# Optimization experiments

Measured on AMD Instinct MI355X. Metric: run time of the kernel, lower is better.

## Reference

```python
import jax, jax.numpy as jnp
import numpy as np

RADIUS = 0.1
NSAMPLE = 32


def _ball_query(new_xyz, xyz, radius, nsample):
    # new_xyz: (B, S, 3), xyz: (B, N, 3) -> idx (B, S, nsample) int32
    N = xyz.shape[1]
    d2 = jnp.sum((new_xyz[:, :, None, :] - xyz[:, None, :, :]) ** 2, axis=-1)  # (B,S,N)
    mask = d2 < radius * radius
    cand = jnp.where(mask, jnp.arange(N, dtype=jnp.int32)[None, None, :], N)
    cand = jnp.sort(cand, axis=-1)[:, :, :nsample]  # first nsample in-ball indices
    first = cand[:, :, :1]
    first = jnp.where(first == N, 0, first)  # empty ball -> index 0 (CUDA semantics)
    return jnp.where(cand == N, first, cand).astype(jnp.int32)


def _group(features, idx):
    # features: (B, C, N), idx: (B, S, K) -> (B, C, S, K)
    return jax.vmap(lambda f, i: f[:, i])(features, idx)


def setup_inputs() -> dict:
    key = jax.random.key(0)
    k1, k2, k3, k4 = jax.random.split(key, 4)
    B, N, S, C = 4, 16384, 2048, 64
    xyz = jax.random.uniform(k1, (B, N, 3), dtype=jnp.float32)
    new_xyz = jax.random.uniform(k2, (B, S, 3), dtype=jnp.float32)
    features = jax.random.normal(k3, (B, C, N), dtype=jnp.float32)
    fps_idx = jax.random.randint(k4, (B, S), 0, N, dtype=jnp.int32)
    return {"xyz": xyz, "new_xyz": new_xyz, "features": features, "fps_idx": fps_idx}


def reference(xyz, new_xyz, features, fps_idx):
    idx = _ball_query(new_xyz, xyz, RADIUS, NSAMPLE)          # (B,S,nsample)
    idx = jnp.concatenate([fps_idx[:, :, None], idx], axis=2)  # (B,S,nsample+1)
    xyz_t = jnp.transpose(xyz, (0, 2, 1))                      # (B,3,N)
    raw_grouped_xyz = _group(xyz_t, idx)                       # (B,3,S,K)
    grouped_xyz = raw_grouped_xyz - jnp.transpose(new_xyz, (0, 2, 1))[..., None]
    grouped_features = _group(features, idx)                   # (B,C,S,K)
    return jnp.concatenate([raw_grouped_xyz, grouped_xyz, grouped_features], axis=1)
```

## Files before the change

kernel.cpp:

```cpp
#include <hip/hip_runtime.h>

#define BB 4
#define NN 16384
#define SS 2048
#define CC 64
#define NS 32
#define KK 33
#define OC 70
#define SCH 4
#define GT 512
#define NC 10
#define NCELL 1000
#define HCAP 224
#define RPAD 0.100001f

__device__ __forceinline__ float sq_nofma(float v) {
  float r = v * v;
  asm volatile("" : "+v"(r));
  return r;
}

__device__ __forceinline__ int cell1(float x) {
  int c = (int)(x * 10.0f);
  return c < 0 ? 0 : (c > 9 ? 9 : c);
}
__device__ __forceinline__ int cell3(float x, float y, float z) {
  return (cell1(z) * NC + cell1(y)) * NC + cell1(x);
}

__device__ __forceinline__ void ball_query_wave(
    const float* __restrict__ xb, float qx, float qy, float qz, int lane,
    int* out) {
  const float R2 = 0.01f;
  int cnt = 0;
  int firstIdx = 0;
  for (int base = 0; base < NN; base += 256) {
    float px[4], py[4], pz[4];
#pragma unroll
    for (int j = 0; j < 4; ++j) {
      int n = base + j * 64 + lane;
      const float* p = xb + n * 3;
      px[j] = p[0]; py[j] = p[1]; pz[j] = p[2];
    }
#pragma unroll
    for (int j = 0; j < 4; ++j) {
      float dx = px[j] - qx, dy = py[j] - qy, dz = pz[j] - qz;
      float d2 = sq_nofma(dx) + sq_nofma(dy);
      asm volatile("" : "+v"(d2));
      d2 = d2 + sq_nofma(dz);
      bool m = d2 < R2;
      unsigned long long bal = __ballot(m);
      if (cnt == 0 && bal) firstIdx = base + j * 64 + __builtin_ctzll(bal);
      int pos = cnt + (int)__popcll(bal & ((1ull << lane) - 1ull));
      if (m && pos < NS) out[pos] = base + j * 64 + lane;
      cnt += (int)__popcll(bal);
    }
    if (cnt >= NS) break;
  }
  if (cnt < NS) {
    int pad = (cnt == 0) ? 0 : firstIdx;
    if (lane >= cnt && lane < NS) out[lane] = pad;
  }
}

__global__ __launch_bounds__(256) void qg_tr_hist2(
    const float* __restrict__ xyz, const float* __restrict__ feat,
    float* __restrict__ featT, int* __restrict__ partial) {
  __shared__ float tile[32 * 260];
  __shared__ int h[1024];
  const int bid = (int)blockIdx.x;
  const int tid = (int)threadIdx.x;
  const int b = bid >> 7;
  const int rest = bid & 127;
  const int n0 = (rest >> 1) << 8;
  const int cc = rest & 1;
  const int c0 = cc << 5;
  const int wv = tid >> 6, lane = tid & 63;

  if (cc == 0) {
#pragma unroll
    for (int c = tid; c < 1024; c += 256) h[c] = 0;
    __syncthreads();
    const float* p = xyz + ((size_t)b * NN + n0 + tid) * 3;
    atomicAdd(&h[cell3(p[0], p[1], p[2])], 1);
  }

  const float* fb = feat + ((size_t)b * CC + c0) * NN + n0;
#pragma unroll
  for (int rr = 0; rr < 8; ++rr) {
    int c = rr * 4 + wv;
    float4 v = *(const float4*)(fb + (size_t)c * NN + 4 * lane);
    *(float4*)&tile[c * 260 + 4 * lane] = v;
  }
  __syncthreads();
  const int c4 = lane & 7, m = lane >> 3;
  float4* oT = (float4*)(featT + ((size_t)b * NN + n0) * CC);
#pragma unroll
  for (int it = 0; it < 8; ++it) {
    int n = it * 32 + wv * 8 + m;
    float4 v;
    v.x = tile[(4 * c4 + 0) * 260 + n];
    v.y = tile[(4 * c4 + 1) * 260 + n];
    v.z = tile[(4 * c4 + 2) * 260 + n];
    v.w = tile[(4 * c4 + 3) * 260 + n];
    oT[(size_t)n * (CC / 4) + (c0 >> 2) + c4] = v;
  }

  if (cc == 0) {
    const int j = rest >> 1;
    int* pr = partial + (((size_t)b * 128 + j) << 10);
#pragma unroll
    for (int c = tid; c < 1024; c += 256) pr[c] = h[c];
  }
}

__global__ __launch_bounds__(256) void qg_scan2(
    const int* __restrict__ partial, int* __restrict__ off,
    int* __restrict__ woff) {
  __shared__ int sc[256];
  const int b = (int)blockIdx.x;
  const int tid = (int)threadIdx.x;
  int l0 = 0, l1 = 0, l2 = 0, l3 = 0;
  for (int j = 0; j < 64; j += 4) {
#pragma unroll
    for (int jj = 0; jj < 4; ++jj) {
      const int4 v = ((const int4*)(partial + (((size_t)b * 128 + j + jj) << 10)))[tid];
      l0 += v.x; l1 += v.y; l2 += v.z; l3 += v.w;
    }
  }
  int base = tid * 4;
  int s1 = l0, s2 = l0 + l1, s3 = l0 + l1 + l2, tot = s3 + l3;
  sc[tid] = tot;
  __syncthreads();
  for (int d = 1; d < 256; d <<= 1) {
    int v = (tid >= d) ? sc[tid - d] : 0;
    __syncthreads();
    sc[tid] += v;
    __syncthreads();
  }
  int ex = sc[tid] - tot;
  int* offb = off + b * (NCELL + 1);
  int* woffb = woff + b * NCELL;
  if (base + 0 < NCELL) { offb[base + 0] = ex;      woffb[base + 0] = ex; }
  if (base + 1 < NCELL) { offb[base + 1] = ex + s1; woffb[base + 1] = ex + s1; }
  if (base + 2 < NCELL) { offb[base + 2] = ex + s2; woffb[base + 2] = ex + s2; }
  if (base + 3 < NCELL) { offb[base + 3] = ex + s3; woffb[base + 3] = ex + s3; }
  if (tid == 0) offb[NCELL] = NN;
}

__global__ __launch_bounds__(256) void qg_scatter(
    const float* __restrict__ xyz, int* __restrict__ woff,
    float4* __restrict__ pts) {
  int i = (int)(blockIdx.x * 256u + threadIdx.x);
  int b = i >> 14, n = i & (NN - 1);
  const float* p = xyz + ((size_t)b * NN + n) * 3;
  float x = p[0], y = p[1], z = p[2];
  int cell = cell3(x, y, z);
  int pos = atomicAdd(&woff[b * NCELL + cell], 1);
  pts[(b << 14) + pos] = make_float4(x, y, z, __int_as_float(n));
}

__global__ __launch_bounds__(GT) void qg_main(
    const float* __restrict__ xyz, const float* __restrict__ nxyz,
    const float4* __restrict__ pts, const int* __restrict__ off,
    const float* __restrict__ featT, const int* __restrict__ fps,
    float* __restrict__ out) {
  __shared__ float sf[CC][SCH * KK + 1];
  __shared__ int sidx[SCH * KK];
  __shared__ int hitbuf[SCH][HCAP];
  __shared__ int hcnt_s[SCH];
  const int tid = (int)threadIdx.x;
  const int blk = (int)blockIdx.x;
  const int b = blk >> 9;
  const int s0 = (blk & 511) * SCH;
  const int wv = tid >> 6, lane = tid & 63;

  if (wv < SCH) {
    const int q = b * SS + s0 + wv;
    const float R2 = 0.01f;
    float qx = nxyz[q * 3 + 0];
    float qy = nxyz[q * 3 + 1];
    float qz = nxyz[q * 3 + 2];
    int* hb = hitbuf[wv];
    int* qout = &sidx[wv * KK];
    if (lane == 0) hcnt_s[wv] = 0;
    asm volatile("s_waitcnt lgkmcnt(0)" ::: "memory");

    int lox = max(0, (int)floorf((qx - RPAD) * 10.f));
    int hix = min(9, (int)floorf((qx + RPAD) * 10.f));
    int loy = max(0, (int)floorf((qy - RPAD) * 10.f));
    int hiy = min(9, (int)floorf((qy + RPAD) * 10.f));
    int loz = max(0, (int)floorf((qz - RPAD) * 10.f));
    int hiz = min(9, (int)floorf((qz + RPAD) * 10.f));

    const int* offb = off + b * (NCELL + 1);
    int start_l = 0, end_l = 0;
    {
      int cz = loz + lane / 3, cy = loy + lane % 3;
      if (lane < 9 && cz <= hiz && cy <= hiy) {
        int row = (cz * NC + cy) * NC;
        start_l = offb[row + lox];
        end_l = offb[row + hix + 1];
      }
    }
    const float4* pb = pts + ((size_t)b << 14);
    for (int sp = 0; sp < 9; ++sp) {
      int start = __shfl(start_l, sp, 64);
      int end = __shfl(end_l, sp, 64);
      for (int p0 = start; p0 < end; p0 += 64) {
        int ii = p0 + lane;
        bool valid = ii < end;
        float4 v = pb[valid ? ii : (end - 1)];
        float dx = v.x - qx, dy = v.y - qy, dz = v.z - qz;
        float d2 = sq_nofma(dx) + sq_nofma(dy);
        asm volatile("" : "+v"(d2));
        d2 = d2 + sq_nofma(dz);
        if (valid && d2 < R2) {
          int pos = atomicAdd(&hcnt_s[wv], 1);
          if (pos < HCAP) hb[pos] = __float_as_int(v.w);
        }
      }
    }
    asm volatile("s_waitcnt lgkmcnt(0)" ::: "memory");
    const int M = hcnt_s[wv];
    if (M > HCAP) {
      ball_query_wave(xyz + (size_t)b * NN * 3, qx, qy, qz, lane, qout + 1);
    } else {
      int minv = 0x7fffffff;
      for (int i = lane; i < M; i += 64) {
        int hh = hb[i];
        minv = min(minv, hh);
        int rank = 0;
        for (int j = 0; j < M; ++j) rank += (hb[j] < hh) ? 1 : 0;
        if (rank < NS) qout[1 + rank] = hh;
      }
      if (M < NS) {
#pragma unroll
        for (int d = 1; d < 64; d <<= 1)
          minv = min(minv, __shfl_xor(minv, d, 64));
        int pad = (M == 0) ? 0 : minv;
        if (lane >= M && lane < NS) qout[1 + lane] = pad;
      }
    }
    if (lane == 0) qout[0] = fps[q];
  }
  __syncthreads();

  const size_t cstr = (size_t)SS * KK;
  const float4* fT4 = (const float4*)(featT + (size_t)b * NN * CC);
  int e = tid & 15;
  for (int pp = tid >> 4; pp < SCH * KK; pp += GT / 16) {
    int n = sidx[pp];
    float4 v = fT4[(size_t)n * (CC / 4) + e];
    sf[4 * e + 0][pp] = v.x;
    sf[4 * e + 1][pp] = v.y;
    sf[4 * e + 2][pp] = v.z;
    sf[4 * e + 3][pp] = v.w;
  }

  if (tid < SCH * KK) {
    int s4 = tid / KK;
    int n = sidx[tid];
    const float* p = xyz + ((size_t)b * NN + n) * 3;
    float x = p[0], y = p[1], z = p[2];
    int q = b * SS + s0 + s4;
    float cx = nxyz[q * 3 + 0], cy = nxyz[q * 3 + 1], cz = nxyz[q * 3 + 2];
    size_t obase = ((size_t)(b * OC) * SS + s0) * KK + tid;
    out[obase + 0 * cstr] = x;
    out[obase + 1 * cstr] = y;
    out[obase + 2 * cstr] = z;
    out[obase + 3 * cstr] = x - cx;
    out[obase + 4 * cstr] = y - cy;
    out[obase + 5 * cstr] = z - cz;
  }
  __syncthreads();

  size_t fbase = ((size_t)(b * OC + 6) * SS + s0) * KK;
  for (int idx = tid; idx < CC * SCH * KK; idx += GT) {
    int c = idx / (SCH * KK);
    int j = idx - c * (SCH * KK);
    out[fbase + (size_t)c * cstr + j] = sf[c][j];
  }
}

__global__ __launch_bounds__(256) void qg_prep(
    const float* __restrict__ xyz, const float* __restrict__ nxyz,
    const float* __restrict__ feat, int* __restrict__ wsidx,
    float* __restrict__ featT) {
  __shared__ float tile[64][65];
  int bid = (int)blockIdx.x;
  int r3 = bid % 3;
  if (r3 < 2) {
    int lane = (int)(threadIdx.x & 63);
    int q = ((bid / 3) * 2 + r3) * 4 + (int)(threadIdx.x >> 6);
    int b = q >> 11;
    const float* xb = xyz + (size_t)b * NN * 3;
    ball_query_wave(xb, nxyz[q * 3], nxyz[q * 3 + 1], nxyz[q * 3 + 2], lane,
                    wsidx + (size_t)q * NS);
  } else {
    int tb = bid / 3;
    int b = tb >> 8;
    int n0 = (tb & 255) << 6;
    int tx = (int)(threadIdx.x & 63);
    int ty = (int)(threadIdx.x >> 6);
    const float* fb = feat + (size_t)b * CC * NN + n0;
#pragma unroll
    for (int r = 0; r < 16; ++r) {
      int c = r * 4 + ty;
      tile[c][tx] = fb[(size_t)c * NN + tx];
    }
    __syncthreads();
    float* ob = featT + ((size_t)b * NN + n0) * CC;
#pragma unroll
    for (int r = 0; r < 16; ++r) {
      int n = r * 4 + ty;
      ob[(size_t)n * CC + tx] = tile[tx][n];
    }
  }
}

__global__ __launch_bounds__(GT) void qg_gather2(
    const float* __restrict__ xyz, const float* __restrict__ nxyz,
    const float* __restrict__ featT, const int* __restrict__ fps,
    const int* __restrict__ wsidx, float* __restrict__ out) {
  __shared__ float sf[CC][SCH * KK + 1];
  __shared__ int sidx[SCH * KK];
  const int tid = (int)threadIdx.x;
  const int blk = (int)blockIdx.x;
  const int b = blk >> 9;
  const int s0 = (blk & 511) * SCH;
  const size_t cstr = (size_t)SS * KK;

  if (tid < SCH * KK) {
    int s4 = tid / KK, k = tid - s4 * KK;
    int q = b * SS + s0 + s4;
    sidx[tid] = (k == 0) ? fps[q] : wsidx[(size_t)q * NS + (k - 1)];
  }
  __syncthreads();

  const float4* fT4 = (const float4*)(featT + (size_t)b * NN * CC);
  int e = tid & 15;
  for (int pp = tid >> 4; pp < SCH * KK; pp += GT / 16) {
    int n = sidx[pp];
    float4 v = fT4[(size_t)n * (CC / 4) + e];
    sf[4 * e + 0][pp] = v.x;
    sf[4 * e + 1][pp] = v.y;
    sf[4 * e + 2][pp] = v.z;
    sf[4 * e + 3][pp] = v.w;
  }

  if (tid < SCH * KK) {
    int s4 = tid / KK;
    int n = sidx[tid];
    const float* p = xyz + ((size_t)b * NN + n) * 3;
    float x = p[0], y = p[1], z = p[2];
    int q = b * SS + s0 + s4;
    float cx = nxyz[q * 3 + 0], cy = nxyz[q * 3 + 1], cz = nxyz[q * 3 + 2];
    size_t obase = ((size_t)(b * OC) * SS + s0) * KK + tid;
    out[obase + 0 * cstr] = x;
    out[obase + 1 * cstr] = y;
    out[obase + 2 * cstr] = z;
    out[obase + 3 * cstr] = x - cx;
    out[obase + 4 * cstr] = y - cy;
    out[obase + 5 * cstr] = z - cz;
  }
  __syncthreads();

  size_t fbase = ((size_t)(b * OC + 6) * SS + s0) * KK;
  for (int idx = tid; idx < CC * SCH * KK; idx += GT) {
    int c = idx / (SCH * KK);
    int j = idx - c * (SCH * KK);
    out[fbase + (size_t)c * cstr + j] = sf[c][j];
  }
}

__global__ __launch_bounds__(256) void qg_ballq(
    const float* __restrict__ xyz, const float* __restrict__ nxyz,
    int* __restrict__ wsidx) {
  int q = (int)((blockIdx.x * blockDim.x + threadIdx.x) >> 6);
  int lane = (int)(threadIdx.x & 63);
  int b = q / SS;
  const float* xb = xyz + (size_t)b * NN * 3;
  ball_query_wave(xb, nxyz[q * 3], nxyz[q * 3 + 1], nxyz[q * 3 + 2], lane,
                  wsidx + (size_t)q * NS);
}

__global__ __launch_bounds__(256) void qg_gather(
    const float* __restrict__ xyz, const float* __restrict__ nxyz,
    const float* __restrict__ feat, const int* __restrict__ fps,
    const int* __restrict__ wsidx, float* __restrict__ out) {
  unsigned t = blockIdx.x * 256u + threadIdx.x;
  const unsigned TOT = (unsigned)BB * OC * SS * KK;
  if (t >= TOT) return;
  unsigned k = t % KK;
  unsigned r = t / KK;
  unsigned s = r % SS;
  r /= SS;
  unsigned c = r % OC;
  unsigned b = r / OC;
  unsigned q = b * SS + s;
  int n = (k == 0) ? fps[q] : wsidx[(size_t)q * NS + (k - 1)];
  float v;
  if (c < 6) {
    unsigned cc = (c < 3) ? c : c - 3;
    v = xyz[((size_t)b * NN + (unsigned)n) * 3 + cc];
    if (c >= 3) v -= nxyz[q * 3 + cc];
  } else {
    v = feat[((size_t)b * CC + (c - 6)) * NN + (unsigned)n];
  }
  out[t] = v;
}

__global__ __launch_bounds__(256) void qg_fused(
    const float* __restrict__ xyz, const float* __restrict__ nxyz,
    const float* __restrict__ feat, const int* __restrict__ fps,
    float* __restrict__ out) {
  __shared__ int sidx[4][KK];
  int wv = (int)(threadIdx.x >> 6), lane = (int)(threadIdx.x & 63);
  int q = (int)blockIdx.x * 4 + wv;
  int b = q / SS, s = q % SS;
  const float* xb = xyz + (size_t)b * NN * 3;
  ball_query_wave(xb, nxyz[q * 3], nxyz[q * 3 + 1], nxyz[q * 3 + 2], lane,
                  &sidx[wv][1]);
  if (lane == 0) sidx[wv][0] = fps[q];
  __syncthreads();
  for (int f = lane; f < OC * KK; f += 64) {
    int c = f / KK, k = f - c * KK;
    int n = sidx[wv][k];
    float v;
    if (c < 6) {
      int cc = (c < 3) ? c : c - 3;
      v = xb[n * 3 + cc];
      if (c >= 3) v -= nxyz[q * 3 + cc];
    } else {
      v = feat[((size_t)b * CC + (c - 6)) * NN + n];
    }
    out[((size_t)((size_t)b * OC + c) * SS + s) * KK + k] = v;
  }
}

extern "C" void kernel_launch(void* const* d_in, const int* in_sizes, int n_in,
                              void* d_out, int out_size, void* d_ws, size_t ws_size,
                              hipStream_t stream) {
  const float* xyz  = (const float*)d_in[0];
  const float* nxyz = (const float*)d_in[1];
  const float* feat = (const float*)d_in[2];
  const int*   fps  = (const int*)d_in[3];
  float* out = (float*)d_out;

  const size_t pts_b     = (size_t)BB * NN * sizeof(float4);
  const size_t off_b     = 16384;
  const size_t partial_b = (size_t)BB * 128 * 1024 * sizeof(int);
  const size_t woff_b    = 16384;
  const size_t featT_b   = (size_t)BB * NN * CC * sizeof(float);
  const size_t grid_need = pts_b + off_b + partial_b + woff_b + featT_b;

  const size_t idx_b = (size_t)BB * SS * NS * sizeof(int);

  if (ws_size >= grid_need) {
    char* w = (char*)d_ws;
    float4* pts     = (float4*)w;                    w += pts_b;
    int*    off     = (int*)w;                       w += off_b;
    int*    partial = (int*)w;                       w += partial_b;
    int*    woff    = (int*)w;                       w += woff_b;
    float*  featT   = (float*)w;
    qg_tr_hist2<<<512, 256, 0, stream>>>(xyz, feat, featT, partial);
    qg_scan2<<<BB, 256, 0, stream>>>(partial, off, woff);
    qg_scatter<<<(BB * NN) / 256, 256, 0, stream>>>(xyz, woff, pts);
    qg_main<<<BB * (SS / SCH), GT, 0, stream>>>(xyz, nxyz, pts, off, featT,
                                                fps, out);
  } else if (ws_size >= idx_b + featT_b) {
    int* wsidx = (int*)d_ws;
    float* featT = (float*)((char*)d_ws + idx_b);
    qg_prep<<<3072, 256, 0, stream>>>(xyz, nxyz, feat, wsidx, featT);
    qg_gather2<<<BB * (SS / SCH), GT, 0, stream>>>(xyz, nxyz, featT, fps,
                                                   wsidx, out);
  } else if (ws_size >= idx_b) {
    int* wsidx = (int*)d_ws;
    qg_ballq<<<(BB * SS) / 4, 256, 0, stream>>>(xyz, nxyz, wsidx);
    unsigned tot = (unsigned)BB * OC * SS * KK;
    qg_gather<<<(tot + 255u) / 256u, 256, 0, stream>>>(xyz, nxyz, feat, fps,
                                                       wsidx, out);
  } else {
    qg_fused<<<(BB * SS) / 4, 256, 0, stream>>>(xyz, nxyz, feat, fps, out);
  }
}
```

Measured before the change: 55.26 us.

## Split fused grid query+gather kernel into separate query and gather kernels

The fused qg_main kernel, which did the cell-grid ball query in 4 of 8 waves and then the feature gather, is split in two. A 256-thread qg_query kernel writes neighbour indices to a new workspace buffer, and the existing qg_gather2 kernel then does the gather. This is meant to stop half the 512-thread block idling during the query and to let each phase run at its own occupancy. The cost is an extra kernel launch plus an index round trip through global memory. The second fallback path also loses the qg_prep route and now uses qg_ballq with qg_gather.

```diff
diff --git a/kernel.cpp b/kernel.cpp
--- a/kernel.cpp
+++ b/kernel.cpp
@@ -160,162 +160,79 @@
   pts[(b << 14) + pos] = make_float4(x, y, z, __int_as_float(n));
 }
 
-__global__ __launch_bounds__(GT) void qg_main(
+__global__ __launch_bounds__(256) void qg_query(
     const float* __restrict__ xyz, const float* __restrict__ nxyz,
     const float4* __restrict__ pts, const int* __restrict__ off,
-    const float* __restrict__ featT, const int* __restrict__ fps,
-    float* __restrict__ out) {
-  __shared__ float sf[CC][SCH * KK + 1];
-  __shared__ int sidx[SCH * KK];
-  __shared__ int hitbuf[SCH][HCAP];
-  __shared__ int hcnt_s[SCH];
+    int* __restrict__ wsidx) {
+  __shared__ int hitbuf[4][HCAP];
+  __shared__ int hcnt_s[4];
   const int tid = (int)threadIdx.x;
-  const int blk = (int)blockIdx.x;
-  const int b = blk >> 9;
-  const int s0 = (blk & 511) * SCH;
   const int wv = tid >> 6, lane = tid & 63;
-
-  if (wv < SCH) {
-    const int q = b * SS + s0 + wv;
-    const float R2 = 0.01f;
-    float qx = nxyz[q * 3 + 0];
-    float qy = nxyz[q * 3 + 1];
-    float qz = nxyz[q * 3 + 2];
-    int* hb = hitbuf[wv];
-    int* qout = &sidx[wv * KK];
-    if (lane == 0) hcnt_s[wv] = 0;
-    asm volatile("s_waitcnt lgkmcnt(0)" ::: "memory");
-
-    int lox = max(0, (int)floorf((qx - RPAD) * 10.f));
-    int hix = min(9, (int)floorf((qx + RPAD) * 10.f));
-    int loy = max(0, (int)floorf((qy - RPAD) * 10.f));
-    int hiy = min(9, (int)floorf((qy + RPAD) * 10.f));
-    int loz = max(0, (int)floorf((qz - RPAD) * 10.f));
-    int hiz = min(9, (int)floorf((qz + RPAD) * 10.f));
-
-    const int* offb = off + b * (NCELL + 1);
-    int start_l = 0, end_l = 0;
-    {
-      int cz = loz + lane / 3, cy = loy + lane % 3;
-      if (lane < 9 && cz <= hiz && cy <= hiy) {
-        int row = (cz * NC + cy) * NC;
-        start_l = offb[row + lox];
-        end_l = offb[row + hix + 1];
+  const int q = (int)blockIdx.x * 4 + wv;
+  const int b = q >> 11;
+  const float R2 = 0.01f;
+  float qx = nxyz[q * 3 + 0];
+  float qy = nxyz[q * 3 + 1];
+  float qz = nxyz[q * 3 + 2];
+  int* hb = hitbuf[wv];
+  int* outp = wsidx + (size_t)q * NS;
+  if (lane == 0) hcnt_s[wv] = 0;
+  asm volatile("s_waitcnt lgkmcnt(0)" ::: "memory");
+
+  int lox = max(0, (int)floorf((qx - RPAD) * 10.f));
+  int hix = min(9, (int)floorf((qx + RPAD) * 10.f));
+  int loy = max(0, (int)floorf((qy - RPAD) * 10.f));
+  int hiy = min(9, (int)floorf((qy + RPAD) * 10.f));
+  int loz = max(0, (int)floorf((qz - RPAD) * 10.f));
+  int hiz = min(9, (int)floorf((qz + RPAD) * 10.f));
+
+  const int* offb = off + b * (NCELL + 1);
+  int start_l = 0, end_l = 0;
+  {
+    int cz = loz + lane / 3, cy = loy + lane % 3;
+    if (lane < 9 && cz <= hiz && cy <= hiy) {
+      int row = (cz * NC + cy) * NC;
+      start_l = offb[row + lox];
+      end_l = offb[row + hix + 1];
+    }
+  }
+  const float4* pb = pts + ((size_t)b << 14);
+  for (int sp = 0; sp < 9; ++sp) {
+    int start = __shfl(start_l, sp, 64);
+    int end = __shfl(end_l, sp, 64);
+    for (int p0 = start; p0 < end; p0 += 64) {
+      int ii = p0 + lane;
+      bool valid = ii < end;
+      float4 v = pb[valid ? ii : (end - 1)];
+      float dx = v.x - qx, dy = v.y - qy, dz = v.z - qz;
+      float d2 = sq_nofma(dx) + sq_nofma(dy);
+      asm volatile("" : "+v"(d2));
+      d2 = d2 + sq_nofma(dz);
+      if (valid && d2 < R2) {
+        int pos = atomicAdd(&hcnt_s[wv], 1);
+        if (pos < HCAP) hb[pos] = __float_as_int(v.w);
       }
     }
-    const float4* pb = pts + ((size_t)b << 14);
-    for (int sp = 0; sp < 9; ++sp) {
-      int start = __shfl(start_l, sp, 64);
-      int end = __shfl(end_l, sp, 64);
-      for (int p0 = start; p0 < end; p0 += 64) {
-        int ii = p0 + lane;
-        bool valid = ii < end;
-        float4 v = pb[valid ? ii : (end - 1)];
-        float dx = v.x - qx, dy = v.y - qy, dz = v.z - qz;
-        float d2 = sq_nofma(dx) + sq_nofma(dy);
-        asm volatile("" : "+v"(d2));
-        d2 = d2 + sq_nofma(dz);
-        if (valid && d2 < R2) {
-          int pos = atomicAdd(&hcnt_s[wv], 1);
-          if (pos < HCAP) hb[pos] = __float_as_int(v.w);
-        }
-      }
-    }
-    asm volatile("s_waitcnt lgkmcnt(0)" ::: "memory");
-    const int M = hcnt_s[wv];
-    if (M > HCAP) {
-      ball_query_wave(xyz + (size_t)b * NN * 3, qx, qy, qz, lane, qout + 1);
-    } else {
-      int minv = 0x7fffffff;
-      for (int i = lane; i < M; i += 64) {
-        int hh = hb[i];
-        minv = min(minv, hh);
-        int rank = 0;
-        for (int j = 0; j < M; ++j) rank += (hb[j] < hh) ? 1 : 0;
-        if (rank < NS) qout[1 + rank] = hh;
-      }
-      if (M < NS) {
-#pragma unroll
-        for (int d = 1; d < 64; d <<= 1)
-          minv = min(minv, __shfl_xor(minv, d, 64));
-        int pad = (M == 0) ? 0 : minv;
-        if (lane >= M && lane < NS) qout[1 + lane] = pad;
-      }
-    }
-    if (lane == 0) qout[0] = fps[q];
-  }
-  __syncthreads();
-
-  const size_t cstr = (size_t)SS * KK;
-  const float4* fT4 = (const float4*)(featT + (size_t)b * NN * CC);
-  int e = tid & 15;
-  for (int pp = tid >> 4; pp < SCH * KK; pp += GT / 16) {
-    int n = sidx[pp];
-    float4 v = fT4[(size_t)n * (CC / 4) + e];
-    sf[4 * e + 0][pp] = v.x;
-    sf[4 * e + 1][pp] = v.y;
-    sf[4 * e + 2][pp] = v.z;
-    sf[4 * e + 3][pp] = v.w;
-  }
-
-  if (tid < SCH * KK) {
-    int s4 = tid / KK;
-    int n = sidx[tid];
-    const float* p = xyz + ((size_t)b * NN + n) * 3;
-    float x = p[0], y = p[1], z = p[2];
-    int q = b * SS + s0 + s4;
-    float cx = nxyz[q * 3 + 0], cy = nxyz[q * 3 + 1], cz = nxyz[q * 3 + 2];
-    size_t obase = ((size_t)(b * OC) * SS + s0) * KK + tid;
-    out[obase + 0 * cstr] = x;
-    out[obase + 1 * cstr] = y;
-    out[obase + 2 * cstr] = z;
-    out[obase + 3 * cstr] = x - cx;
-    out[obase + 4 * cstr] = y - cy;
-    out[obase + 5 * cstr] = z - cz;
-  }
-  __syncthreads();
-
-  size_t fbase = ((size_t)(b * OC + 6) * SS + s0) * KK;
-  for (int idx = tid; idx < CC * SCH * KK; idx += GT) {
-    int c = idx / (SCH * KK);
-    int j = idx - c * (SCH * KK);
-    out[fbase + (size_t)c * cstr + j] = sf[c][j];
-  }
-}
-
-__global__ __launch_bounds__(256) void qg_prep(
-    const float* __restrict__ xyz, const float* __restrict__ nxyz,
-    const float* __restrict__ feat, int* __restrict__ wsidx,
-    float* __restrict__ featT) {
-  __shared__ float tile[64][65];
-  int bid = (int)blockIdx.x;
-  int r3 = bid % 3;
-  if (r3 < 2) {
-    int lane = (int)(threadIdx.x & 63);
-    int q = ((bid / 3) * 2 + r3) * 4 + (int)(threadIdx.x >> 6);
-    int b = q >> 11;
-    const float* xb = xyz + (size_t)b * NN * 3;
-    ball_query_wave(xb, nxyz[q * 3], nxyz[q * 3 + 1], nxyz[q * 3 + 2], lane,
-                    wsidx + (size_t)q * NS);
-  } else {
-    int tb = bid / 3;
-    int b = tb >> 8;
-    int n0 = (tb & 255) << 6;
-    int tx = (int)(threadIdx.x & 63);
-    int ty = (int)(threadIdx.x >> 6);
-    const float* fb = feat + (size_t)b * CC * NN + n0;
-#pragma unroll
-    for (int r = 0; r < 16; ++r) {
-      int c = r * 4 + ty;
-      tile[c][tx] = fb[(size_t)c * NN + tx];
-    }
-    __syncthreads();
-    float* ob = featT + ((size_t)b * NN + n0) * CC;
-#pragma unroll
-    for (int r = 0; r < 16; ++r) {
-      int n = r * 4 + ty;
-      ob[(size_t)n * CC + tx] = tile[tx][n];
-    }
+  }
+  asm volatile("s_waitcnt lgkmcnt(0)" ::: "memory");
+  const int M = hcnt_s[wv];
+  if (M > HCAP) {
+    ball_query_wave(xyz + (size_t)b * NN * 3, qx, qy, qz, lane, outp);
+    return;
+  }
+  int minv = 0x7fffffff;
+  for (int i = lane; i < M; i += 64) {
+    int hh = hb[i];
+    minv = min(minv, hh);
+    int rank = 0;
+    for (int j = 0; j < M; ++j) rank += (hb[j] < hh) ? 1 : 0;
+    if (rank < NS) outp[rank] = hh;
+  }
+  if (M < NS) {
+#pragma unroll
+    for (int d = 1; d < 64; d <<= 1) minv = min(minv, __shfl_xor(minv, d, 64));
+    int pad = (M == 0) ? 0 : minv;
+    if (lane >= M && lane < NS) outp[lane] = pad;
   }
 }
 
@@ -452,10 +369,9 @@
   const size_t off_b     = 16384;
   const size_t partial_b = (size_t)BB * 128 * 1024 * sizeof(int);
   const size_t woff_b    = 16384;
+  const size_t idx_b     = (size_t)BB * SS * NS * sizeof(int);
   const size_t featT_b   = (size_t)BB * NN * CC * sizeof(float);
-  const size_t grid_need = pts_b + off_b + partial_b + woff_b + featT_b;
-
-  const size_t idx_b = (size_t)BB * SS * NS * sizeof(int);
+  const size_t grid_need = pts_b + off_b + partial_b + woff_b + idx_b + featT_b;
 
   if (ws_size >= grid_need) {
     char* w = (char*)d_ws;
@@ -463,18 +379,21 @@
     int*    off     = (int*)w;                       w += off_b;
     int*    partial = (int*)w;                       w += partial_b;
     int*    woff    = (int*)w;                       w += woff_b;
+    int*    wsidx   = (int*)w;                       w += idx_b;
     float*  featT   = (float*)w;
     qg_tr_hist2<<<512, 256, 0, stream>>>(xyz, feat, featT, partial);
     qg_scan2<<<BB, 256, 0, stream>>>(partial, off, woff);
     qg_scatter<<<(BB * NN) / 256, 256, 0, stream>>>(xyz, woff, pts);
-    qg_main<<<BB * (SS / SCH), GT, 0, stream>>>(xyz, nxyz, pts, off, featT,
-                                                fps, out);
+    qg_query<<<(BB * SS) / 4, 256, 0, stream>>>(xyz, nxyz, pts, off, wsidx);
+    qg_gather2<<<BB * (SS / SCH), GT, 0, stream>>>(xyz, nxyz, featT, fps,
+                                                   wsidx, out);
   } else if (ws_size >= idx_b + featT_b) {
     int* wsidx = (int*)d_ws;
     float* featT = (float*)((char*)d_ws + idx_b);
-    qg_prep<<<3072, 256, 0, stream>>>(xyz, nxyz, feat, wsidx, featT);
-    qg_gather2<<<BB * (SS / SCH), GT, 0, stream>>>(xyz, nxyz, featT, fps,
-                                                   wsidx, out);
+    qg_ballq<<<(BB * SS) / 4, 256, 0, stream>>>(xyz, nxyz, wsidx);
+    unsigned tot = (unsigned)BB * OC * SS * KK;
+    qg_gather<<<(tot + 255u) / 256u, 256, 0, stream>>>(xyz, nxyz, feat, fps,
+                                                       wsidx, out);
   } else if (ws_size >= idx_b) {
     int* wsidx = (int*)d_ws;
     qg_ballq<<<(BB * SS) / 4, 256, 0, stream>>>(xyz, nxyz, wsidx);
```

After: 59.65 us. +7.9%, slower.
